# Kernel tuning notes

Hardware: AMD Instinct MI355X
Metric: run time of the kernel (lower is better)

The kernel has to match this reference:

```python
import jax, jax.numpy as jnp
import numpy as np
import math

D_MODEL = 1024
N_HEADS = 16
SEQ = 2048
BATCH = 2


def setup_inputs() -> dict:
    key = jax.random.key(0)
    ks = jax.random.split(key, 7)
    scale = 1.0 / math.sqrt(D_MODEL)
    return {
        "q": jax.random.normal(ks[0], (SEQ, BATCH, D_MODEL), jnp.float32),
        "k": jax.random.normal(ks[1], (SEQ, BATCH, D_MODEL), jnp.float32),
        "v": jax.random.normal(ks[2], (SEQ, BATCH, D_MODEL), jnp.float32),
        "in_proj_w": jax.random.normal(ks[3], (3 * D_MODEL, D_MODEL), jnp.float32) * scale,
        "in_proj_b": jax.random.normal(ks[4], (3 * D_MODEL,), jnp.float32) * 0.01,
        "out_proj_w": jax.random.normal(ks[5], (D_MODEL, D_MODEL), jnp.float32) * scale,
        "out_proj_b": jax.random.normal(ks[6], (D_MODEL,), jnp.float32) * 0.01,
    }


def reference(q, k, v, in_proj_w, in_proj_b, out_proj_w, out_proj_b):
    # q, k, v: (S, B, D) seq-first layout as in the torch module
    S, B, D = q.shape
    H = N_HEADS
    dk = D // H
    wq, wk, wv = jnp.split(in_proj_w, 3, axis=0)   # each (D, D)
    bq, bk, bv = jnp.split(in_proj_b, 3, axis=0)   # each (D,)
    qp = q @ wq.T + bq
    kp = k @ wk.T + bk
    vp = v @ wv.T + bv
    # (S, B, D) -> (S, B*H, dk) -> (B*H, S, dk)
    def to_heads(x, s):
        return x.reshape(s, B * H, dk).transpose(1, 0, 2)
    qh = to_heads(qp, S)
    kh = to_heads(kp, k.shape[0])
    vh = to_heads(vp, v.shape[0])
    # scores: (B*H, Sq, Sk)
    scores = jnp.einsum('bqd,bkd->bqk', qh, kh) / math.sqrt(dk)
    probs = jax.nn.softmax(scores, axis=-1)
    attn = jnp.einsum('bqk,bkd->bqd', probs, vh)   # (B*H, S, dk)
    # (B*H, S, dk) -> (S, B*H, dk) -> (S*B, D)
    attn = attn.transpose(1, 0, 2).reshape(S * B, D)
    out = attn @ out_proj_w.T + out_proj_b
    return out.reshape(S, B, D)
```

## Files before the change

### kernel.cpp

```cpp
#include <hip/hip_runtime.h>
#include <math.h>

#define SEQ    2048
#define BATCH  2
#define DMODEL 1024
#define NHEADS 16
#define DK     64

typedef __attribute__((ext_vector_type(8))) short  bf16x8;
typedef __attribute__((ext_vector_type(4))) float  f32x4;
typedef __attribute__((ext_vector_type(8))) unsigned short u16x8;

#define GLD16(gp, lp) __builtin_amdgcn_global_load_lds(                      \
    (__attribute__((address_space(1))) void*)(gp),                            \
    (__attribute__((address_space(3))) void*)(lp), 16, 0, 0)

__device__ inline unsigned short f2bf(float f) {
    unsigned int u = __float_as_uint(f);
    u += 0x7fffu + ((u >> 16) & 1u);
    return (unsigned short)(u >> 16);
}

__device__ inline float fast_exp2(float x) {
#if __has_builtin(__builtin_amdgcn_exp2f)
    return __builtin_amdgcn_exp2f(x);
#else
    return __expf(x * 0.69314718055994531f);
#endif
}

#define WS_QB   0u
#define WS_KB   4194304u
#define WS_VB   8388608u
#define WS_WIB  12582912u
#define WS_WOB  15728640u
#define WS_QH   16777216u
#define WS_KH   20971520u
#define WS_VT   25165824u
#define WS_ATT  29360128u

__global__ __launch_bounds__(256) void cast_all_kernel(
    const float* __restrict__ q, const float* __restrict__ k,
    const float* __restrict__ v, const float* __restrict__ w_in,
    const float* __restrict__ w_out, unsigned short* __restrict__ ws)
{
    const int gid = blockIdx.x * 256 + threadIdx.x;
    const float* src; unsigned short* dst;
    if (gid < 524288)       { int g = gid;           src = q     + (size_t)g*8; dst = ws + WS_QB  + (size_t)g*8; }
    else if (gid < 1048576) { int g = gid - 524288;  src = k     + (size_t)g*8; dst = ws + WS_KB  + (size_t)g*8; }
    else if (gid < 1572864) { int g = gid - 1048576; src = v     + (size_t)g*8; dst = ws + WS_VB  + (size_t)g*8; }
    else if (gid < 1966080) { int g = gid - 1572864; src = w_in  + (size_t)g*8; dst = ws + WS_WIB + (size_t)g*8; }
    else                    { int g = gid - 1966080; src = w_out + (size_t)g*8; dst = ws + WS_WOB + (size_t)g*8; }
    float4 a = *(const float4*)src;
    float4 b = *(const float4*)(src + 4);
    u16x8 o;
    o[0]=f2bf(a.x); o[1]=f2bf(a.y); o[2]=f2bf(a.z); o[3]=f2bf(a.w);
    o[4]=f2bf(b.x); o[5]=f2bf(b.y); o[6]=f2bf(b.z); o[7]=f2bf(b.w);
    *(u16x8*)dst = o;
}

__global__ __launch_bounds__(256) void qkv_gemm_kernel(
    const unsigned short* __restrict__ ws_in, const float* __restrict__ bias,
    unsigned short* __restrict__ ws_out)
{
    __shared__ unsigned short As[128*32];
    __shared__ unsigned short Bs[128*32];

    const int t    = threadIdx.x;
    const int lane = t & 63;
    const int w    = t >> 6;
    const int lrow = lane & 15;
    const int quad = lane >> 4;
    const int wm   = (w >> 1) * 64;
    const int wn   = (w & 1) * 64;

    const int n0    = blockIdx.x * 128;
    const int m0    = blockIdx.y * 128;
    const int which = n0 >> 10;

    const unsigned short* A = ws_in + WS_QB + (size_t)which * 4194304u;
    const unsigned short* B = ws_in + WS_WIB;

    const int srow = t >> 2;
    const int scc  = (t & 3) ^ ((t >> 3) & 3);
    const unsigned short* gA0 = A + (size_t)(m0 + srow) * 1024 + scc * 8;
    const unsigned short* gA1 = A + (size_t)(m0 + 64 + srow) * 1024 + scc * 8;
    const unsigned short* gB0 = B + (size_t)(n0 + srow) * 1024 + scc * 8;
    const unsigned short* gB1 = B + (size_t)(n0 + 64 + srow) * 1024 + scc * 8;

    f32x4 acc[4][4] = {};

    #pragma unroll 1
    for (int kt = 0; kt < 1024; kt += 32) {
        __syncthreads();
        GLD16(gA0, As + (size_t)t * 8);
        GLD16(gA1, As + (size_t)(t + 256) * 8);
        GLD16(gB0, Bs + (size_t)t * 8);
        GLD16(gB1, Bs + (size_t)(t + 256) * 8);
        gA0 += 32; gA1 += 32; gB0 += 32; gB1 += 32;
        __syncthreads();

        bf16x8 af[4], bf[4];
        #pragma unroll
        for (int mt = 0; mt < 4; ++mt) {
            const int r = wm + mt*16 + lrow;
            af[mt] = *(const bf16x8*)(As + r*32 + ((quad ^ ((r>>1)&3))*8));
        }
        #pragma unroll
        for (int nt = 0; nt < 4; ++nt) {
            const int r = wn + nt*16 + lrow;
            bf[nt] = *(const bf16x8*)(Bs + r*32 + ((quad ^ ((r>>1)&3))*8));
        }
        #pragma unroll
        for (int mt = 0; mt < 4; ++mt)
            #pragma unroll
            for (int nt = 0; nt < 4; ++nt)
                acc[mt][nt] = __builtin_amdgcn_mfma_f32_16x16x32_bf16(
                    af[mt], bf[nt], acc[mt][nt], 0, 0, 0);
    }

    unsigned short* dstQK = ws_out + WS_QH + (size_t)which * 4194304u;
    unsigned short* dstV  = ws_out + WS_VT;
    const float qscale = 0.18033688011112042f;

    #pragma unroll
    for (int nt = 0; nt < 4; ++nt) {
        const int n = n0 + wn + nt*16 + lrow;
        const float bn = bias[n];
        const int h = (n & 1023) >> 6;
        const int d = n & 63;
        #pragma unroll
        for (int mt = 0; mt < 4; ++mt) {
            if (which < 2) {
                #pragma unroll
                for (int r = 0; r < 4; ++r) {
                    const int m = m0 + wm + mt*16 + quad*4 + r;
                    const int s = m >> 1, b = m & 1;
                    float val = acc[mt][nt][r] + bn;
                    if (which == 0) val *= qscale;
                    dstQK[((size_t)((b<<4) + h) * 2048 + s) * 64 + d] = f2bf(val);
                }
            } else {
                const int m_base = m0 + wm + mt*16 + quad*4;
                const int s0 = m_base >> 1;
                unsigned int pk0 = (unsigned int)f2bf(acc[mt][nt][0] + bn)
                                 | ((unsigned int)f2bf(acc[mt][nt][2] + bn) << 16);
                unsigned int pk1 = (unsigned int)f2bf(acc[mt][nt][1] + bn)
                                 | ((unsigned int)f2bf(acc[mt][nt][3] + bn) << 16);
                *(unsigned int*)(dstV + ((size_t)h*64 + d)*2048 + s0)        = pk0;
                *(unsigned int*)(dstV + ((size_t)(16 + h)*64 + d)*2048 + s0) = pk1;
            }
        }
    }
}

__global__ __launch_bounds__(256, 4) void attn_mfma_kernel(
    const unsigned short* __restrict__ qh, const unsigned short* __restrict__ kh,
    const unsigned short* __restrict__ vt, unsigned short* __restrict__ attn)
{
    __shared__ unsigned short Qs[64*64];
    __shared__ unsigned short Ks[64*64];
    __shared__ unsigned short Vts[64*64];
    __shared__ unsigned short Ps[64*64];

    const int t    = threadIdx.x;
    const int lane = t & 63;
    const int w    = t >> 6;
    const int lrow = lane & 15;
    const int quad = lane >> 4;

    const int qt = blockIdx.x;
    const int bh = blockIdx.y;

    const unsigned short* Qg = qh + ((size_t)bh * 2048 + qt * 64) * 64;
    const unsigned short* Kb = kh + (size_t)bh * 2048 * 64;
    const unsigned short* Vb = vt + (size_t)bh * 64 * 2048;

    #pragma unroll
    for (int i = 0; i < 2; ++i) {
        const int c = i*256 + t;
        const int row = c >> 3, cc = c & 7;
        GLD16(Qg + (size_t)row*64 + ((cc ^ (row & 7))*8), Qs + (size_t)c*8);
    }

    f32x4 O[4] = {};
    float m_i[4], l_i[4];
    #pragma unroll
    for (int r = 0; r < 4; ++r) { m_i[r] = -INFINITY; l_i[r] = 0.f; }

    #pragma unroll 1
    for (int ktile = 0; ktile < 32; ++ktile) {
        __syncthreads();
        const unsigned short* Kg = Kb + (size_t)ktile * 64 * 64;
        const unsigned short* Vg = Vb + (size_t)ktile * 64;
        #pragma unroll
        for (int i = 0; i < 2; ++i) {
            const int c = i*256 + t;
            const int row = c >> 3, cc = (c & 7) ^ (row & 7);
            GLD16(Kg + (size_t)row*64   + cc*8, Ks  + (size_t)c*8);
            GLD16(Vg + (size_t)row*2048 + cc*8, Vts + (size_t)c*8);
        }
        __syncthreads();

        f32x4 S[4] = {};
        #pragma unroll
        for (int kk = 0; kk < 2; ++kk) {
            const int qrow = w*16 + lrow;
            bf16x8 aq = *(const bf16x8*)(Qs + qrow*64 + (((kk*4+quad) ^ (qrow&7))*8));
            #pragma unroll
            for (int nt = 0; nt < 4; ++nt) {
                const int krow = nt*16 + lrow;
                bf16x8 bk = *(const bf16x8*)(Ks + krow*64 + (((kk*4+quad) ^ (krow&7))*8));
                S[nt] = __builtin_amdgcn_mfma_f32_16x16x32_bf16(aq, bk, S[nt], 0, 0, 0);
            }
        }

        float mx[4];
        int anynew = 0;
        #pragma unroll
        for (int r = 0; r < 4; ++r) {
            float m = fmaxf(fmaxf(S[0][r], S[1][r]), fmaxf(S[2][r], S[3][r]));
            #pragma unroll
            for (int off = 1; off <= 8; off <<= 1)
                m = fmaxf(m, __shfl_xor(m, off, 64));
            mx[r] = m;
            anynew |= (m > m_i[r]);
        }

        const int prow_base = w*16 + quad*4;
        if (__any(anynew)) {
            #pragma unroll
            for (int r = 0; r < 4; ++r) {
                const float mn = fmaxf(m_i[r], mx[r]);
                const float al = fast_exp2(m_i[r] - mn);
                m_i[r] = mn;
                float rsum = 0.f;
                const int prow = prow_base + r;
                const int pb = prow * 64;
                #pragma unroll
                for (int nt = 0; nt < 4; ++nt) {
                    const float p = fast_exp2(S[nt][r] - mn);
                    const int c = nt*2 + (lrow >> 3);
                    Ps[pb + ((c ^ (prow & 7))*8) + (lrow & 7)] = f2bf(p);
                    rsum += p;
                }
                #pragma unroll
                for (int off = 1; off <= 8; off <<= 1)
                    rsum += __shfl_xor(rsum, off, 64);
                l_i[r] = l_i[r]*al + rsum;
                #pragma unroll
                for (int dt = 0; dt < 4; ++dt) O[dt][r] *= al;
            }
        } else {
            #pragma unroll
            for (int r = 0; r < 4; ++r) {
                const float mn = m_i[r];
                float rsum = 0.f;
                const int prow = prow_base + r;
                const int pb = prow * 64;
                #pragma unroll
                for (int nt = 0; nt < 4; ++nt) {
                    const float p = fast_exp2(S[nt][r] - mn);
                    const int c = nt*2 + (lrow >> 3);
                    Ps[pb + ((c ^ (prow & 7))*8) + (lrow & 7)] = f2bf(p);
                    rsum += p;
                }
                #pragma unroll
                for (int off = 1; off <= 8; off <<= 1)
                    rsum += __shfl_xor(rsum, off, 64);
                l_i[r] += rsum;
            }
        }

        #pragma unroll
        for (int kk = 0; kk < 2; ++kk) {
            const int prow = w*16 + lrow;
            bf16x8 ap = *(const bf16x8*)(Ps + prow*64 + (((kk*4+quad) ^ (prow&7))*8));
            #pragma unroll
            for (int dt = 0; dt < 4; ++dt) {
                const int vrow = dt*16 + lrow;
                bf16x8 bv = *(const bf16x8*)(Vts + vrow*64 + (((kk*4+quad) ^ (vrow&7))*8));
                O[dt] = __builtin_amdgcn_mfma_f32_16x16x32_bf16(ap, bv, O[dt], 0, 0, 0);
            }
        }
    }

    const int b_ = bh >> 4, h_ = bh & 15;
    #pragma unroll
    for (int r = 0; r < 4; ++r) {
        const float inv = 1.f / l_i[r];
        const int s_ = qt*64 + w*16 + quad*4 + r;
        #pragma unroll
        for (int dt = 0; dt < 4; ++dt) {
            attn[((size_t)(s_*2 + b_)) * 1024 + h_*64 + dt*16 + lrow] =
                f2bf(O[dt][r] * inv);
        }
    }
}

__global__ __launch_bounds__(256) void out_gemm_kernel(
    const unsigned short* __restrict__ A, const unsigned short* __restrict__ B,
    const float* __restrict__ bias, float* __restrict__ out)
{
    __shared__ unsigned short As[64*32];
    __shared__ unsigned short Bs[128*32];

    const int t    = threadIdx.x;
    const int lane = t & 63;
    const int w    = t >> 6;
    const int lrow = lane & 15;
    const int quad = lane >> 4;
    const int wn   = (w >> 1) * 64;
    const int wm   = (w & 1) * 32;

    const int n0 = blockIdx.x * 128;
    const int m0 = blockIdx.y * 64;

    const int srow = t >> 2;
    const int scc  = (t & 3) ^ ((t >> 3) & 3);
    const unsigned short* gA0 = A + (size_t)(m0 + srow) * 1024 + scc * 8;
    const unsigned short* gB0 = B + (size_t)(n0 + srow) * 1024 + scc * 8;
    const unsigned short* gB1 = B + (size_t)(n0 + 64 + srow) * 1024 + scc * 8;

    f32x4 acc[2][4] = {};

    #pragma unroll 1
    for (int kt = 0; kt < 1024; kt += 32) {
        __syncthreads();
        GLD16(gA0, As + (size_t)t * 8);
        GLD16(gB0, Bs + (size_t)t * 8);
        GLD16(gB1, Bs + (size_t)(t + 256) * 8);
        gA0 += 32; gB0 += 32; gB1 += 32;
        __syncthreads();

        bf16x8 af[2], bf[4];
        #pragma unroll
        for (int mt = 0; mt < 2; ++mt) {
            const int r = wm + mt*16 + lrow;
            af[mt] = *(const bf16x8*)(As + r*32 + ((quad ^ ((r>>1)&3))*8));
        }
        #pragma unroll
        for (int nt = 0; nt < 4; ++nt) {
            const int r = wn + nt*16 + lrow;
            bf[nt] = *(const bf16x8*)(Bs + r*32 + ((quad ^ ((r>>1)&3))*8));
        }
        #pragma unroll
        for (int mt = 0; mt < 2; ++mt)
            #pragma unroll
            for (int nt = 0; nt < 4; ++nt)
                acc[mt][nt] = __builtin_amdgcn_mfma_f32_16x16x32_bf16(
                    af[mt], bf[nt], acc[mt][nt], 0, 0, 0);
    }

    #pragma unroll
    for (int nt = 0; nt < 4; ++nt) {
        const int n = n0 + wn + nt*16 + lrow;
        const float bn = bias[n];
        #pragma unroll
        for (int mt = 0; mt < 2; ++mt) {
            #pragma unroll
            for (int r = 0; r < 4; ++r) {
                const int m = m0 + wm + mt*16 + quad*4 + r;
                out[(size_t)m * 1024 + n] = acc[mt][nt][r] + bn;
            }
        }
    }
}

extern "C" void kernel_launch(void* const* d_in, const int* in_sizes, int n_in,
                              void* d_out, int out_size, void* d_ws, size_t ws_size,
                              hipStream_t stream) {
    const float* q     = (const float*)d_in[0];
    const float* k     = (const float*)d_in[1];
    const float* v     = (const float*)d_in[2];
    const float* w_in  = (const float*)d_in[3];
    const float* b_in  = (const float*)d_in[4];
    const float* w_out = (const float*)d_in[5];
    const float* b_out = (const float*)d_in[6];
    float* out = (float*)d_out;

    unsigned short* ws = (unsigned short*)d_ws;

    cast_all_kernel<<<8192, 256, 0, stream>>>(q, k, v, w_in, w_out, ws);
    qkv_gemm_kernel<<<dim3(24, 32), 256, 0, stream>>>(ws, b_in, ws);
    attn_mfma_kernel<<<dim3(32, 32), 256, 0, stream>>>(
        ws + WS_QH, ws + WS_KH, ws + WS_VT, ws + WS_ATT);
    out_gemm_kernel<<<dim3(8, 64), 256, 0, stream>>>(
        ws + WS_ATT, ws + WS_WOB, b_out, out);
}
```

Before: 279.5 us.

## Restructure attention to 2 waves of 32 query rows with transposed S tile

The attention kernel now runs 128 threads per block, with each wave owning 32 query rows instead of 16. It computes S transposed (K as the A operand, Q as the B operand) so each lane holds whole rows for the max and sum reductions, which cuts the shuffle count, and it writes P and the output as packed bf16 pairs through a hardware pack-convert intrinsic. The aim is more MFMA reuse of each K and V fragment load from LDS and less reduction overhead. The trade-off is fewer waves per block, higher register pressure, and the loss of the occupancy hint from launch bounds.

```diff
diff --git a/kernel.cpp b/kernel.cpp
--- a/kernel.cpp
+++ b/kernel.cpp
@@ -19,6 +19,16 @@
     unsigned int u = __float_as_uint(f);
     u += 0x7fffu + ((u >> 16) & 1u);
     return (unsigned short)(u >> 16);
+}
+
+__device__ inline unsigned int pk2bf(float a, float b) {
+#if __has_builtin(__builtin_amdgcn_cvt_pk_bf16_f32)
+    typedef __attribute__((ext_vector_type(2))) __bf16 v2bf;
+    v2bf r = __builtin_amdgcn_cvt_pk_bf16_f32(a, b);
+    unsigned int u; __builtin_memcpy(&u, &r, 4); return u;
+#else
+    return (unsigned int)f2bf(a) | ((unsigned int)f2bf(b) << 16);
+#endif
 }
 
 __device__ inline float fast_exp2(float x) {
@@ -143,10 +153,8 @@
             } else {
                 const int m_base = m0 + wm + mt*16 + quad*4;
                 const int s0 = m_base >> 1;
-                unsigned int pk0 = (unsigned int)f2bf(acc[mt][nt][0] + bn)
-                                 | ((unsigned int)f2bf(acc[mt][nt][2] + bn) << 16);
-                unsigned int pk1 = (unsigned int)f2bf(acc[mt][nt][1] + bn)
-                                 | ((unsigned int)f2bf(acc[mt][nt][3] + bn) << 16);
+                unsigned int pk0 = pk2bf(acc[mt][nt][0] + bn, acc[mt][nt][2] + bn);
+                unsigned int pk1 = pk2bf(acc[mt][nt][1] + bn, acc[mt][nt][3] + bn);
                 *(unsigned int*)(dstV + ((size_t)h*64 + d)*2048 + s0)        = pk0;
                 *(unsigned int*)(dstV + ((size_t)(16 + h)*64 + d)*2048 + s0) = pk1;
             }
@@ -154,7 +162,7 @@
     }
 }
 
-__global__ __launch_bounds__(256, 4) void attn_mfma_kernel(
+__global__ __launch_bounds__(128) void attn_mfma_kernel(
     const unsigned short* __restrict__ qh, const unsigned short* __restrict__ kh,
     const unsigned short* __restrict__ vt, unsigned short* __restrict__ attn)
 {
@@ -177,16 +185,14 @@
     const unsigned short* Vb = vt + (size_t)bh * 64 * 2048;
 
     #pragma unroll
-    for (int i = 0; i < 2; ++i) {
-        const int c = i*256 + t;
-        const int row = c >> 3, cc = c & 7;
-        GLD16(Qg + (size_t)row*64 + ((cc ^ (row & 7))*8), Qs + (size_t)c*8);
-    }
-
-    f32x4 O[4] = {};
-    float m_i[4], l_i[4];
-    #pragma unroll
-    for (int r = 0; r < 4; ++r) { m_i[r] = -INFINITY; l_i[r] = 0.f; }
+    for (int i = 0; i < 4; ++i) {
+        const int c = i*128 + t;
+        const int row = c >> 3, cc = (c & 7) ^ (row & 7);
+        GLD16(Qg + (size_t)row*64 + cc*8, Qs + (size_t)c*8);
+    }
+
+    f32x4 O[4][2] = {};
+    float m_i[2] = {-INFINITY, -INFINITY}, l_i[2] = {0.f, 0.f};
 
     #pragma unroll 1
     for (int ktile = 0; ktile < 32; ++ktile) {
@@ -194,106 +200,126 @@
         const unsigned short* Kg = Kb + (size_t)ktile * 64 * 64;
         const unsigned short* Vg = Vb + (size_t)ktile * 64;
         #pragma unroll
-        for (int i = 0; i < 2; ++i) {
-            const int c = i*256 + t;
+        for (int i = 0; i < 4; ++i) {
+            const int c = i*128 + t;
             const int row = c >> 3, cc = (c & 7) ^ (row & 7);
             GLD16(Kg + (size_t)row*64   + cc*8, Ks  + (size_t)c*8);
             GLD16(Vg + (size_t)row*2048 + cc*8, Vts + (size_t)c*8);
         }
         __syncthreads();
 
-        f32x4 S[4] = {};
+        f32x4 ST[4][2] = {};
         #pragma unroll
         for (int kk = 0; kk < 2; ++kk) {
-            const int qrow = w*16 + lrow;
-            bf16x8 aq = *(const bf16x8*)(Qs + qrow*64 + (((kk*4+quad) ^ (qrow&7))*8));
-            #pragma unroll
-            for (int nt = 0; nt < 4; ++nt) {
-                const int krow = nt*16 + lrow;
-                bf16x8 bk = *(const bf16x8*)(Ks + krow*64 + (((kk*4+quad) ^ (krow&7))*8));
-                S[nt] = __builtin_amdgcn_mfma_f32_16x16x32_bf16(aq, bk, S[nt], 0, 0, 0);
-            }
-        }
-
-        float mx[4];
+            bf16x8 kf[4], qf[2];
+            #pragma unroll
+            for (int m = 0; m < 4; ++m) {
+                const int r = m*16 + lrow;
+                kf[m] = *(const bf16x8*)(Ks + r*64 + (((kk*4+quad) ^ (r&7))*8));
+            }
+            #pragma unroll
+            for (int n = 0; n < 2; ++n) {
+                const int r = w*32 + n*16 + lrow;
+                qf[n] = *(const bf16x8*)(Qs + r*64 + (((kk*4+quad) ^ (r&7))*8));
+            }
+            #pragma unroll
+            for (int m = 0; m < 4; ++m)
+                #pragma unroll
+                for (int n = 0; n < 2; ++n)
+                    ST[m][n] = __builtin_amdgcn_mfma_f32_16x16x32_bf16(
+                        kf[m], qf[n], ST[m][n], 0, 0, 0);
+        }
+
+        float mx[2], al[2];
         int anynew = 0;
         #pragma unroll
-        for (int r = 0; r < 4; ++r) {
-            float m = fmaxf(fmaxf(S[0][r], S[1][r]), fmaxf(S[2][r], S[3][r]));
-            #pragma unroll
-            for (int off = 1; off <= 8; off <<= 1)
-                m = fmaxf(m, __shfl_xor(m, off, 64));
-            mx[r] = m;
-            anynew |= (m > m_i[r]);
-        }
-
-        const int prow_base = w*16 + quad*4;
+        for (int n = 0; n < 2; ++n) {
+            float mm;
+            #pragma unroll
+            for (int m = 0; m < 4; ++m) {
+                float m01 = fmaxf(fmaxf(ST[m][n][0], ST[m][n][1]),
+                                  fmaxf(ST[m][n][2], ST[m][n][3]));
+                mm = (m == 0) ? m01 : fmaxf(mm, m01);
+            }
+            mm = fmaxf(mm, __shfl_xor(mm, 16, 64));
+            mm = fmaxf(mm, __shfl_xor(mm, 32, 64));
+            mx[n] = mm;
+            anynew |= (mm > m_i[n]);
+        }
+
         if (__any(anynew)) {
             #pragma unroll
-            for (int r = 0; r < 4; ++r) {
-                const float mn = fmaxf(m_i[r], mx[r]);
-                const float al = fast_exp2(m_i[r] - mn);
-                m_i[r] = mn;
-                float rsum = 0.f;
-                const int prow = prow_base + r;
-                const int pb = prow * 64;
+            for (int n = 0; n < 2; ++n) {
+                const float mn = fmaxf(m_i[n], mx[n]);
+                al[n] = fast_exp2(m_i[n] - mn);
+                m_i[n] = mn;
+            }
+            #pragma unroll
+            for (int dt = 0; dt < 4; ++dt)
                 #pragma unroll
-                for (int nt = 0; nt < 4; ++nt) {
-                    const float p = fast_exp2(S[nt][r] - mn);
-                    const int c = nt*2 + (lrow >> 3);
-                    Ps[pb + ((c ^ (prow & 7))*8) + (lrow & 7)] = f2bf(p);
-                    rsum += p;
-                }
+                for (int n = 0; n < 2; ++n)
+                    O[dt][n] *= al[n];
+        } else {
+            al[0] = 1.f; al[1] = 1.f;
+        }
+
+        #pragma unroll
+        for (int n = 0; n < 2; ++n) {
+            const int prow = w*32 + n*16 + lrow;
+            const float mn = m_i[n];
+            float rsum = 0.f;
+            #pragma unroll
+            for (int m = 0; m < 4; ++m) {
+                const float p0 = fast_exp2(ST[m][n][0] - mn);
+                const float p1 = fast_exp2(ST[m][n][1] - mn);
+                const float p2 = fast_exp2(ST[m][n][2] - mn);
+                const float p3 = fast_exp2(ST[m][n][3] - mn);
+                rsum += (p0 + p1) + (p2 + p3);
+                uint2 pk;
+                pk.x = pk2bf(p0, p1);
+                pk.y = pk2bf(p2, p3);
+                const int sc = (m*2 + (quad >> 1)) ^ (prow & 7);
+                *(uint2*)(Ps + prow*64 + sc*8 + (quad & 1)*4) = pk;
+            }
+            rsum += __shfl_xor(rsum, 16, 64);
+            rsum += __shfl_xor(rsum, 32, 64);
+            l_i[n] = l_i[n]*al[n] + rsum;
+        }
+
+        #pragma unroll
+        for (int kk = 0; kk < 2; ++kk) {
+            bf16x8 vf[4], pf[2];
+            #pragma unroll
+            for (int dt = 0; dt < 4; ++dt) {
+                const int r = dt*16 + lrow;
+                vf[dt] = *(const bf16x8*)(Vts + r*64 + (((kk*4+quad) ^ (r&7))*8));
+            }
+            #pragma unroll
+            for (int n = 0; n < 2; ++n) {
+                const int r = w*32 + n*16 + lrow;
+                pf[n] = *(const bf16x8*)(Ps + r*64 + (((kk*4+quad) ^ (r&7))*8));
+            }
+            #pragma unroll
+            for (int dt = 0; dt < 4; ++dt)
                 #pragma unroll
-                for (int off = 1; off <= 8; off <<= 1)
-                    rsum += __shfl_xor(rsum, off, 64);
-                l_i[r] = l_i[r]*al + rsum;
-                #pragma unroll
-                for (int dt = 0; dt < 4; ++dt) O[dt][r] *= al;
-            }
-        } else {
-            #pragma unroll
-            for (int r = 0; r < 4; ++r) {
-                const float mn = m_i[r];
-                float rsum = 0.f;
-                const int prow = prow_base + r;
-                const int pb = prow * 64;
-                #pragma unroll
-                for (int nt = 0; nt < 4; ++nt) {
-                    const float p = fast_exp2(S[nt][r] - mn);
-                    const int c = nt*2 + (lrow >> 3);
-                    Ps[pb + ((c ^ (prow & 7))*8) + (lrow & 7)] = f2bf(p);
-                    rsum += p;
-                }
-                #pragma unroll
-                for (int off = 1; off <= 8; off <<= 1)
-                    rsum += __shfl_xor(rsum, off, 64);
-                l_i[r] += rsum;
-            }
-        }
-
-        #pragma unroll
-        for (int kk = 0; kk < 2; ++kk) {
-            const int prow = w*16 + lrow;
-            bf16x8 ap = *(const bf16x8*)(Ps + prow*64 + (((kk*4+quad) ^ (prow&7))*8));
-            #pragma unroll
-            for (int dt = 0; dt < 4; ++dt) {
-                const int vrow = dt*16 + lrow;
-                bf16x8 bv = *(const bf16x8*)(Vts + vrow*64 + (((kk*4+quad) ^ (vrow&7))*8));
-                O[dt] = __builtin_amdgcn_mfma_f32_16x16x32_bf16(ap, bv, O[dt], 0, 0, 0);
-            }
+                for (int n = 0; n < 2; ++n)
+                    O[dt][n] = __builtin_amdgcn_mfma_f32_16x16x32_bf16(
+                        vf[dt], pf[n], O[dt][n], 0, 0, 0);
         }
     }
 
     const int b_ = bh >> 4, h_ = bh & 15;
     #pragma unroll
-    for (int r = 0; r < 4; ++r) {
-        const float inv = 1.f / l_i[r];
-        const int s_ = qt*64 + w*16 + quad*4 + r;
+    for (int n = 0; n < 2; ++n) {
+        const float inv = 1.f / l_i[n];
+        const int s_ = qt*64 + w*32 + n*16 + lrow;
+        unsigned short* dst = attn + ((size_t)(s_*2 + b_)) * 1024 + h_*64;
         #pragma unroll
         for (int dt = 0; dt < 4; ++dt) {
-            attn[((size_t)(s_*2 + b_)) * 1024 + h_*64 + dt*16 + lrow] =
-                f2bf(O[dt][r] * inv);
+            uint2 pk;
+            pk.x = pk2bf(O[dt][n][0]*inv, O[dt][n][1]*inv);
+            pk.y = pk2bf(O[dt][n][2]*inv, O[dt][n][3]*inv);
+            *(uint2*)(dst + dt*16 + quad*4) = pk;
         }
     }
 }
@@ -383,7 +409,7 @@
 
     cast_all_kernel<<<8192, 256, 0, stream>>>(q, k, v, w_in, w_out, ws);
     qkv_gemm_kernel<<<dim3(24, 32), 256, 0, stream>>>(ws, b_in, ws);
-    attn_mfma_kernel<<<dim3(32, 32), 256, 0, stream>>>(
+    attn_mfma_kernel<<<dim3(32, 32), 128, 0, stream>>>(
         ws + WS_QH, ws + WS_KH, ws + WS_VT, ws + WS_ATT);
     out_gemm_kernel<<<dim3(8, 64), 256, 0, stream>>>(
         ws + WS_ATT, ws + WS_WOB, b_out, out);
```

Measured after the change: 252.4 us. 1.11x faster.
